# Kernel optimization log

Measured on AMD Instinct MI355X. Metric: run time of the kernel, lower is better.

The kernel has to match this reference:

```python
import jax, jax.numpy as jnp
import numpy as np

N = 50000      # nodes
E = 800000     # edges
IN = 128       # in_dim
EMB = 32       # emb_dim
ED = 8         # edge_dim
L = 4          # num_layers
B = 64         # num graphs in batch
OUT = 10       # out_dim
EPS = 1e-5


def setup_inputs() -> dict:
    key = jax.random.key(0)
    ks = jax.random.split(key, 16)
    f32 = jnp.float32
    def nrm(k, shape, scale):
        return jax.random.normal(k, shape, dtype=f32) * scale
    inp = {}
    inp['x'] = nrm(ks[0], (N, IN), 1.0)
    inp['edge_index'] = jax.random.randint(ks[1], (2, E), 0, N)
    inp['edge_attr'] = nrm(ks[2], (E, ED), 1.0)
    inp['batch'] = jnp.sort(jax.random.randint(ks[3], (N,), 0, B))
    # lin_in
    inp['lin_in_w'] = nrm(ks[4], (IN, EMB), 0.05)
    inp['lin_in_b'] = jnp.zeros((EMB,), f32)
    # per-layer message MLP: Linear(2e+ed->e), BN, ReLU, Linear(e->e), BN, ReLU
    inp['msg_w1'] = nrm(ks[5], (L, 2 * EMB + ED, EMB), 0.1)
    inp['msg_b1'] = jnp.zeros((L, EMB), f32)
    inp['msg_g1'] = jnp.ones((L, EMB), f32)
    inp['msg_be1'] = jnp.zeros((L, EMB), f32)
    inp['msg_w2'] = nrm(ks[6], (L, EMB, EMB), 0.1)
    inp['msg_b2'] = jnp.zeros((L, EMB), f32)
    inp['msg_g2'] = jnp.ones((L, EMB), f32)
    inp['msg_be2'] = jnp.zeros((L, EMB), f32)
    # per-layer update MLP: Linear(2e->e), BN, ReLU, Linear(e->e), BN, ReLU
    inp['upd_w1'] = nrm(ks[7], (L, 2 * EMB, EMB), 0.1)
    inp['upd_b1'] = jnp.zeros((L, EMB), f32)
    inp['upd_g1'] = jnp.ones((L, EMB), f32)
    inp['upd_be1'] = jnp.zeros((L, EMB), f32)
    inp['upd_w2'] = nrm(ks[8], (L, EMB, EMB), 0.1)
    inp['upd_b2'] = jnp.zeros((L, EMB), f32)
    inp['upd_g2'] = jnp.ones((L, EMB), f32)
    inp['upd_be2'] = jnp.zeros((L, EMB), f32)
    # lin_pred
    inp['pred_w'] = nrm(ks[9], (EMB, OUT), 0.1)
    inp['pred_b'] = jnp.zeros((OUT,), f32)
    return inp


def _bn(x, g, b):
    # BatchNorm1d in training mode: batch stats over dim 0 (biased variance)
    mu = jnp.mean(x, axis=0)
    var = jnp.mean(jnp.square(x - mu), axis=0)
    return (x - mu) * jax.lax.rsqrt(var + EPS) * g + b


def reference(x, edge_attr, lin_in_w, lin_in_b,
              msg_w1, msg_b1, msg_g1, msg_be1, msg_w2, msg_b2, msg_g2, msg_be2,
              upd_w1, upd_b1, upd_g1, upd_be1, upd_w2, upd_b2, upd_g2, upd_be2,
              pred_w, pred_b, edge_index, batch):
    src = edge_index[0]  # h_j source nodes
    dst = edge_index[1]  # h_i target nodes (aggregation index)
    h = x @ lin_in_w + lin_in_b  # [N, EMB]
    for i in range(L):
        # message: gather + concat + MLP(BN,ReLU)x2 over edges
        msg_in = jnp.concatenate([h[dst], h[src], edge_attr], axis=-1)  # [E, 2e+ed]
        m = jax.nn.relu(_bn(msg_in @ msg_w1[i] + msg_b1[i], msg_g1[i], msg_be1[i]))
        m = jax.nn.relu(_bn(m @ msg_w2[i] + msg_b2[i], msg_g2[i], msg_be2[i]))
        # aggregate: scatter-add by destination
        aggr = jax.ops.segment_sum(m, dst, num_segments=N)  # [N, EMB]
        # update: concat + MLP(BN,ReLU)x2
        u = jnp.concatenate([h, aggr], axis=-1)  # [N, 2e]
        u = jax.nn.relu(_bn(u @ upd_w1[i] + upd_b1[i], upd_g1[i], upd_be1[i]))
        u = jax.nn.relu(_bn(u @ upd_w2[i] + upd_b2[i], upd_g2[i], upd_be2[i]))
        h = u + h  # residual in MPNNModel.get_embeddings
    # global mean pool
    sums = jax.ops.segment_sum(h, batch, num_segments=B)
    counts = jax.ops.segment_sum(jnp.ones((N,), h.dtype), batch, num_segments=B)
    h_graph = sums / jnp.maximum(counts, 1.0)[:, None]
    return h_graph @ pred_w + pred_b  # [B, OUT]
```

## Files before the change

### kernel.cpp

```cpp
#include <hip/hip_runtime.h>
#include <cstddef>

#define N_NODES 50000
#define N_EDGES 800000
#define IN_DIM  128
#define EMB     32
#define ED      8
#define NLAYERS 4
#define NB      64
#define OUTD    10
#define EPS_BN  1e-5f

#define EDGE_GRID 3125
#define NODE_GRID 196
#define NODE4_GRID 782
#define AU_GRID   6250
#define MSG1_EPT  2
#define MSG1_GRID 1563
#define NCHUNK    12500
#define MSG12_CPW 4
#define MSG12_GRID 782
#define NTILE_N   3125
#define LIN_GRID  782
#define SREP 4

typedef short bf16x8 __attribute__((ext_vector_type(8)));
typedef float f32x4  __attribute__((ext_vector_type(4)));


__device__ __forceinline__ unsigned short f2bf(float x) {
  union { float f; unsigned u; } v; v.f = x;
  unsigned b = v.u + 0x7FFFu + ((v.u >> 16) & 1u);
  return (unsigned short)(b >> 16);
}
__device__ __forceinline__ float bf2f(unsigned short s) {
  union { unsigned u; float f; } v; v.u = ((unsigned)s) << 16;
  return v.f;
}

__device__ __forceinline__ void coef_from_stats(const float* __restrict__ stats_stage,
                                                const float* __restrict__ g,
                                                const float* __restrict__ be,
                                                float inv_count, float* __restrict__ cf) {
  if (threadIdx.x < EMB) {
    const int c = threadIdx.x;
    float s = 0.f, ss = 0.f;
#pragma unroll
    for (int r = 0; r < SREP; ++r) {
      s  += stats_stage[r*64 + c];
      ss += stats_stage[r*64 + EMB + c];
    }
    const float mu  = s * inv_count;
    const float var = ss * inv_count - mu*mu;
    const float a = g[c] * rsqrtf(var + EPS_BN);
    cf[c] = a;
    cf[EMB + c] = fmaf(-mu, a, be[c]);
  }
  __syncthreads();
}

__device__ __forceinline__ void block_stats_atomic(const float ts[EMB], const float tss[EMB],
                                                   float* __restrict__ stats_stage) {
  __shared__ float sred[256];
  const int lane = threadIdx.x & 63;
  const int wid  = threadIdx.x >> 6;
#pragma unroll
  for (int c = 0; c < EMB; ++c) {
    float a = ts[c];
    float q = tss[c];
#pragma unroll
    for (int o = 32; o > 0; o >>= 1) {
      a += __shfl_down(a, o, 64);
      q += __shfl_down(q, o, 64);
    }
    if (lane == 0) { sred[wid*64 + c] = a; sred[wid*64 + EMB + c] = q; }
  }
  __syncthreads();
  if (threadIdx.x < 64) {
    const float v = sred[threadIdx.x] + sred[64 + threadIdx.x] +
                    sred[128 + threadIdx.x] + sred[192 + threadIdx.x];
    atomicAdd(stats_stage + ((blockIdx.x & (SREP-1)) << 6) + threadIdx.x, v);
  }
}

__device__ __forceinline__ void wave_stats_atomic(float ts[8], float tss[8],
                                                  float* __restrict__ lds_s,
                                                  float* __restrict__ lds_q,
                                                  float* __restrict__ stats_stage) {
  const int lane = threadIdx.x & 63;
  const int wv   = threadIdx.x >> 6;
#pragma unroll
  for (int j = 0; j < 8; ++j) {
    float a = ts[j], b = tss[j];
#pragma unroll
    for (int o = 32; o > 0; o >>= 1) {
      a += __shfl_down(a, o, 64);
      b += __shfl_down(b, o, 64);
    }
    ts[j] = a; tss[j] = b;
  }
  if (lane == 0) {
#pragma unroll
    for (int j = 0; j < 8; ++j) {
      lds_s[wv*8 + j] = ts[j];
      lds_q[wv*8 + j] = tss[j];
    }
  }
  __syncthreads();
  if (threadIdx.x < 64) {
    const float v = (threadIdx.x < 32) ? lds_s[threadIdx.x] : lds_q[threadIdx.x - 32];
    atomicAdd(stats_stage + ((blockIdx.x & (SREP-1)) << 6) + threadIdx.x, v);
  }
}

__device__ __forceinline__ void y1_compute(float acc[EMB],
    const unsigned short* __restrict__ pb, const unsigned short* __restrict__ qb,
    int dst, int src, const unsigned short* __restrict__ ea_perm, int i,
    const float* __restrict__ w1b) {
  const uint4* pd = (const uint4*)(pb + (size_t)dst*EMB);
  const uint4* qs = (const uint4*)(qb + (size_t)src*EMB);
#pragma unroll
  for (int j4 = 0; j4 < 4; ++j4) {
    const uint4 a = pd[j4];
    const uint4 b = qs[j4];
    const unsigned ua[4] = {a.x, a.y, a.z, a.w};
    const unsigned ub[4] = {b.x, b.y, b.z, b.w};
#pragma unroll
    for (int t = 0; t < 4; ++t) {
      acc[j4*8 + 2*t]   = bf2f((unsigned short)(ua[t] & 0xFFFFu)) +
                          bf2f((unsigned short)(ub[t] & 0xFFFFu));
      acc[j4*8 + 2*t+1] = bf2f((unsigned short)(ua[t] >> 16)) +
                          bf2f((unsigned short)(ub[t] >> 16));
    }
  }
  const uint4 eraw = *(const uint4*)(ea_perm + (size_t)i*ED);
  const unsigned ue[4] = {eraw.x, eraw.y, eraw.z, eraw.w};
  float ev[8];
#pragma unroll
  for (int t = 0; t < 4; ++t) {
    ev[2*t]   = bf2f((unsigned short)(ue[t] & 0xFFFFu));
    ev[2*t+1] = bf2f((unsigned short)(ue[t] >> 16));
  }
#pragma unroll
  for (int k = 0; k < 8; ++k) {
    const float* wk = w1b + k*EMB;
#pragma unroll
    for (int c = 0; c < EMB; ++c) acc[c] = fmaf(ev[k], wk[c], acc[c]);
  }
}

#define HSTRIDE 40

__global__ __launch_bounds__(256) void k_lin_in_pq(
    const float* __restrict__ x, const float* __restrict__ w, const float* __restrict__ b,
    const float* __restrict__ w1, const float* __restrict__ b1, const int* __restrict__ ei,
    float* __restrict__ h, unsigned short* __restrict__ p, unsigned short* __restrict__ q,
    int* __restrict__ cnt)
{
  __shared__ __align__(16) unsigned short lds_hb[4][16*HSTRIDE];
  __shared__ __align__(16) unsigned short lds_pq[4][16*HSTRIDE];
  const int lane = threadIdx.x & 63;
  const int wv   = threadIdx.x >> 6;
  const int n0i  = lane & 15;
  const int quad = lane >> 4;

  const int tile = blockIdx.x*4 + wv;
  if (tile < NTILE_N) {
    const int r0 = tile*16;
    bf16x8 BwL[4], BwH[4];
#pragma unroll
    for (int kb = 0; kb < 4; ++kb) {
#pragma unroll
      for (int j = 0; j < 8; ++j) {
        const int k = kb*32 + quad*8 + j;
        BwL[kb][j] = (short)f2bf(w[k*EMB + n0i]);
        BwH[kb][j] = (short)f2bf(w[k*EMB + 16 + n0i]);
      }
    }
    f32x4 accL = {0.f,0.f,0.f,0.f};
    f32x4 accH = {0.f,0.f,0.f,0.f};
#pragma unroll
    for (int kb = 0; kb < 4; ++kb) {
      const float4 xa = *(const float4*)(x + (size_t)(r0 + n0i)*IN_DIM + kb*32 + quad*8);
      const float4 xb = *(const float4*)(x + (size_t)(r0 + n0i)*IN_DIM + kb*32 + quad*8 + 4);
      bf16x8 A;
      A[0] = (short)f2bf(xa.x); A[1] = (short)f2bf(xa.y);
      A[2] = (short)f2bf(xa.z); A[3] = (short)f2bf(xa.w);
      A[4] = (short)f2bf(xb.x); A[5] = (short)f2bf(xb.y);
      A[6] = (short)f2bf(xb.z); A[7] = (short)f2bf(xb.w);
      accL = __builtin_amdgcn_mfma_f32_16x16x32_bf16(A, BwL[kb], accL, 0, 0, 0);
      accH = __builtin_amdgcn_mfma_f32_16x16x32_bf16(A, BwH[kb], accH, 0, 0, 0);
    }
    const float bL = b[n0i], bH = b[16 + n0i];
#pragma unroll
    for (int r = 0; r < 4; ++r) {
      const int row = quad*4 + r;
      const float vL = accL[r] + bL;
      const float vH = accH[r] + bH;
      h[(size_t)(r0 + row)*EMB + n0i]      = vL;
      h[(size_t)(r0 + row)*EMB + 16 + n0i] = vH;
      lds_hb[wv][row*HSTRIDE + n0i]      = f2bf(vL);
      lds_hb[wv][row*HSTRIDE + 16 + n0i] = f2bf(vH);
    }
    bf16x8 A2;
#pragma unroll
    for (int j = 0; j < 8; ++j)
      A2[j] = (short)lds_hb[wv][n0i*HSTRIDE + quad*8 + j];
    bf16x8 BpL, BpH, BqL, BqH;
#pragma unroll
    for (int j = 0; j < 8; ++j) {
      const int k = quad*8 + j;
      BpL[j] = (short)f2bf(w1[k*EMB + n0i]);
      BpH[j] = (short)f2bf(w1[k*EMB + 16 + n0i]);
      BqL[j] = (short)f2bf(w1[(EMB + k)*EMB + n0i]);
      BqH[j] = (short)f2bf(w1[(EMB + k)*EMB + 16 + n0i]);
    }
    const f32x4 z4 = {0.f,0.f,0.f,0.f};
    f32x4 pL = __builtin_amdgcn_mfma_f32_16x16x32_bf16(A2, BpL, z4, 0, 0, 0);
    f32x4 pH = __builtin_amdgcn_mfma_f32_16x16x32_bf16(A2, BpH, z4, 0, 0, 0);
    f32x4 qL = __builtin_amdgcn_mfma_f32_16x16x32_bf16(A2, BqL, z4, 0, 0, 0);
    f32x4 qH = __builtin_amdgcn_mfma_f32_16x16x32_bf16(A2, BqH, z4, 0, 0, 0);
    const float b1L = b1[n0i], b1H = b1[16 + n0i];
#pragma unroll
    for (int r = 0; r < 4; ++r) {
      const int row = quad*4 + r;
      lds_pq[wv][row*HSTRIDE + n0i]      = f2bf(pL[r] + b1L);
      lds_pq[wv][row*HSTRIDE + 16 + n0i] = f2bf(pH[r] + b1H);
    }
    {
      const int row2 = lane >> 2;
      const int c8   = (lane & 3)*8;
      const uint4 ov = *(const uint4*)&lds_pq[wv][row2*HSTRIDE + c8];
      *(uint4*)(p + (size_t)(r0 + row2)*EMB + c8) = ov;
    }
#pragma unroll
    for (int r = 0; r < 4; ++r) {
      const int row = quad*4 + r;
      lds_pq[wv][row*HSTRIDE + n0i]      = f2bf(qL[r]);
      lds_pq[wv][row*HSTRIDE + 16 + n0i] = f2bf(qH[r]);
    }
    {
      const int row2 = lane >> 2;
      const int c8   = (lane & 3)*8;
      const uint4 ov = *(const uint4*)&lds_pq[wv][row2*HSTRIDE + c8];
      *(uint4*)(q + (size_t)(r0 + row2)*EMB + c8) = ov;
    }
  }
  for (int e = blockIdx.x*256 + threadIdx.x; e < N_EDGES; e += gridDim.x*256)
    atomicAdd(&cnt[ei[N_EDGES + e]], 1);
}

__global__ __launch_bounds__(256) void k_scan_a(const int* __restrict__ cnt,
                                                int* __restrict__ row_ptr, int* __restrict__ bsum) {
  __shared__ int s[256];
  const int gid = blockIdx.x*256 + threadIdx.x;
  const int v = (gid < N_NODES) ? cnt[gid] : 0;
  s[threadIdx.x] = v;
  __syncthreads();
  for (int o = 1; o < 256; o <<= 1) {
    const int t = (threadIdx.x >= o) ? s[threadIdx.x - o] : 0;
    __syncthreads();
    s[threadIdx.x] += t;
    __syncthreads();
  }
  if (gid < N_NODES) row_ptr[gid] = s[threadIdx.x] - v;
  if (threadIdx.x == 255) bsum[blockIdx.x] = s[255];
}

__global__ __launch_bounds__(256) void k_scan_bc(int* __restrict__ row_ptr,
                                                 const int* __restrict__ bsum) {
  __shared__ int s[256];
  const int t = threadIdx.x;
  const int v = (t < NODE_GRID) ? bsum[t] : 0;
  s[t] = v;
  __syncthreads();
  for (int o = 1; o < 256; o <<= 1) {
    const int tt = (t >= o) ? s[t - o] : 0;
    __syncthreads();
    s[t] += tt;
    __syncthreads();
  }
  const int off = (blockIdx.x == 0) ? 0 : s[blockIdx.x - 1];
  const int gid = blockIdx.x*256 + t;
  if (gid < N_NODES) row_ptr[gid] += off;
  if (blockIdx.x == 0 && t == 0) row_ptr[N_NODES] = N_EDGES;
}

__global__ __launch_bounds__(256) void k_place(const int* __restrict__ ei,
                                               const int* __restrict__ row_ptr,
                                               int* __restrict__ cnt2, int* __restrict__ perm) {
  const int e = blockIdx.x*256 + threadIdx.x;
  const int d = ei[N_EDGES + e];
  const int pos = row_ptr[d] + atomicAdd(&cnt2[d], 1);
  perm[pos] = e;
}

__global__ __launch_bounds__(256) void k_permute(
    const int* __restrict__ perm, const int* __restrict__ ei, const float* __restrict__ ea,
    int* __restrict__ src_perm, int* __restrict__ dst_perm, unsigned short* __restrict__ ea_perm)
{
  const int i = blockIdx.x*256 + threadIdx.x;
  const int e = perm[i];
  src_perm[i] = ei[e];
  dst_perm[i] = ei[N_EDGES + e];
  const float4 v0 = ((const float4*)(ea + (size_t)e*ED))[0];
  const float4 v1 = ((const float4*)(ea + (size_t)e*ED))[1];
  const float ev[8] = {v0.x, v0.y, v0.z, v0.w, v1.x, v1.y, v1.z, v1.w};
  unsigned u[4];
#pragma unroll
  for (int j = 0; j < 4; ++j)
    u[j] = (unsigned)f2bf(ev[2*j]) | ((unsigned)f2bf(ev[2*j+1]) << 16);
  uint4 o; o.x = u[0]; o.y = u[1]; o.z = u[2]; o.w = u[3];
  *(uint4*)(ea_perm + (size_t)i*ED) = o;
}


__global__ __launch_bounds__(256) void k_msg1_stats(
    const unsigned short* __restrict__ pb, const unsigned short* __restrict__ qb,
    const int* __restrict__ src_perm, const int* __restrict__ dst_perm,
    const unsigned short* __restrict__ ea_perm,
    const float* __restrict__ w1b, float* __restrict__ stats)
{
  float ts[EMB], tss[EMB];
#pragma unroll
  for (int c = 0; c < EMB; ++c) { ts[c] = 0.f; tss[c] = 0.f; }
  const int base = blockIdx.x*(256*MSG1_EPT) + threadIdx.x;
  for (int it = 0; it < MSG1_EPT; ++it) {
    const int i = base + it*256;
    if (i >= N_EDGES) break;
    float acc[EMB];
    y1_compute(acc, pb, qb, dst_perm[i], src_perm[i], ea_perm, i, w1b);
#pragma unroll
    for (int c = 0; c < EMB; ++c) {
      ts[c] += acc[c];
      tss[c] = fmaf(acc[c], acc[c], tss[c]);
    }
  }
  block_stats_atomic(ts, tss, stats);
}

#define MSTRIDE 40
__global__ __launch_bounds__(256) void k_msg12(
    const unsigned short* __restrict__ pb, const unsigned short* __restrict__ qb,
    const int* __restrict__ src_perm, const int* __restrict__ dst_perm,
    const unsigned short* __restrict__ ea_perm,
    const float* __restrict__ w1b,
    const float* __restrict__ stats1, const float* __restrict__ g1, const float* __restrict__ be1,
    const float* __restrict__ w2, const float* __restrict__ b2,
    unsigned short* __restrict__ y, float* __restrict__ stats2)
{
  __shared__ __align__(16) unsigned short lds_a[4][64*MSTRIDE];
  __shared__ float lds_s[4][32], lds_q[4][32];
  __shared__ float cf[64];

  coef_from_stats(stats1, g1, be1, 1.0f/(float)N_EDGES, cf);

  const int lane = threadIdx.x & 63;
  const int wv   = threadIdx.x >> 6;
  const int n0i  = lane & 15;
  const int kb   = lane >> 4;

  bf16x8 Blo, Bhi;
#pragma unroll
  for (int j = 0; j < 8; ++j) {
    Blo[j] = (short)f2bf(w2[(kb*8 + j)*EMB + n0i]);
    Bhi[j] = (short)f2bf(w2[(kb*8 + j)*EMB + 16 + n0i]);
  }
  const float b2c0 = b2[n0i], b2c1 = b2[16 + n0i];
  float a1[EMB], c1[EMB];
#pragma unroll
  for (int c = 0; c < EMB; ++c) { a1[c] = cf[c]; c1[c] = cf[EMB + c]; }

  float ts[8], tss[8];
#pragma unroll
  for (int j = 0; j < 8; ++j) { ts[j] = 0.f; tss[j] = 0.f; }

  const int chunk0 = (blockIdx.x*4 + wv)*MSG12_CPW;
  for (int cix = 0; cix < MSG12_CPW; ++cix) {
    const int chunk = chunk0 + cix;
    if (chunk >= NCHUNK) break;
    const size_t e0 = (size_t)chunk*64;
    const int i = (int)e0 + lane;

    {
      float acc[EMB];
      y1_compute(acc, pb, qb, dst_perm[i], src_perm[i], ea_perm, i, w1b);
      unsigned u[16];
#pragma unroll
      for (int j = 0; j < 16; ++j) {
        const float v0 = fmaxf(fmaf(a1[2*j],   acc[2*j],   c1[2*j]),   0.f);
        const float v1 = fmaxf(fmaf(a1[2*j+1], acc[2*j+1], c1[2*j+1]), 0.f);
        u[j] = (unsigned)f2bf(v0) | ((unsigned)f2bf(v1) << 16);
      }
      uint4* row = (uint4*)&lds_a[wv][lane*MSTRIDE];
#pragma unroll
      for (int j = 0; j < 4; ++j) {
        uint4 o; o.x = u[4*j]; o.y = u[4*j+1]; o.z = u[4*j+2]; o.w = u[4*j+3];
        row[j] = o;
      }
    }
#pragma unroll
    for (int t = 0; t < 4; ++t) {
      const uint4 araw = *(const uint4*)&lds_a[wv][(16*t + n0i)*MSTRIDE + kb*8];
      bf16x8 A;
      const unsigned ua[4] = {araw.x, araw.y, araw.z, araw.w};
#pragma unroll
      for (int j = 0; j < 4; ++j) {
        A[2*j]   = (short)(ua[j] & 0xFFFFu);
        A[2*j+1] = (short)(ua[j] >> 16);
      }
      f32x4 acc0 = {0.f, 0.f, 0.f, 0.f};
      f32x4 acc1 = {0.f, 0.f, 0.f, 0.f};
      acc0 = __builtin_amdgcn_mfma_f32_16x16x32_bf16(A, Blo, acc0, 0, 0, 0);
      acc1 = __builtin_amdgcn_mfma_f32_16x16x32_bf16(A, Bhi, acc1, 0, 0, 0);
#pragma unroll
      for (int r = 0; r < 4; ++r) {
        const int row = 16*t + kb*4 + r;
        lds_a[wv][row*MSTRIDE + n0i]      = f2bf(acc0[r] + b2c0);
        lds_a[wv][row*MSTRIDE + 16 + n0i] = f2bf(acc1[r] + b2c1);
      }
    }
#pragma unroll
    for (int j = 0; j < 4; ++j) {
      const int c64 = lane + 64*j;
      const int row = c64 >> 2;
      const int c8  = (c64 & 3)*8;
      const uint4 ov = *(const uint4*)&lds_a[wv][row*MSTRIDE + c8];
      *(uint4*)(y + (e0 + row)*EMB + c8) = ov;
      const unsigned uo[4] = {ov.x, ov.y, ov.z, ov.w};
#pragma unroll
      for (int jj = 0; jj < 4; ++jj) {
        const float v0 = bf2f((unsigned short)(uo[jj] & 0xFFFFu));
        const float v1 = bf2f((unsigned short)(uo[jj] >> 16));
        ts[2*jj]   += v0;  tss[2*jj]   = fmaf(v0, v0, tss[2*jj]);
        ts[2*jj+1] += v1;  tss[2*jj+1] = fmaf(v1, v1, tss[2*jj+1]);
      }
    }
  }

#pragma unroll
  for (int j = 0; j < 8; ++j) {
    float s = ts[j], qq = tss[j];
#pragma unroll
    for (int o = 4; o < 64; o <<= 1) {
      s  += __shfl_xor(s, o, 64);
      qq += __shfl_xor(qq, o, 64);
    }
    ts[j] = s; tss[j] = qq;
  }
  if (lane < 4) {
#pragma unroll
    for (int j = 0; j < 8; ++j) {
      lds_s[wv][lane*8 + j] = ts[j];
      lds_q[wv][lane*8 + j] = tss[j];
    }
  }
  __syncthreads();
  if (threadIdx.x < 64) {
    const int c = threadIdx.x & 31;
    const int kind = threadIdx.x >> 5;
    float v = 0.f;
#pragma unroll
    for (int wq = 0; wq < 4; ++wq)
      v += kind ? lds_q[wq][c] : lds_s[wq][c];
    atomicAdd(stats2 + ((blockIdx.x & (SREP-1)) << 6) + kind*32 + c, v);
  }
}

__global__ __launch_bounds__(256) void k_aggr_upd1(
    const unsigned short* __restrict__ y, const int* __restrict__ row_ptr,
    const float* __restrict__ h,
    const float* __restrict__ stats1, const float* __restrict__ g2, const float* __restrict__ be2,
    const float* __restrict__ uw1, const float* __restrict__ ub1,
    float* __restrict__ z, float* __restrict__ stats2)
{
  __shared__ float cf[64];
  __shared__ float lh[8][32];
  __shared__ float la[8][32];
  __shared__ float rs[4][32], rq[4][32];
  coef_from_stats(stats1, g2, be2, 1.0f/(float)N_EDGES, cf);

  const int g = threadIdx.x >> 5;
  const int l = threadIdx.x & 31;
  const int n = blockIdx.x*8 + g;

  lh[g][l] = h[(size_t)n*EMB + l];

  const int rof = l >> 4;
  const int cp  = l & 15;
  const float a0 = cf[2*cp],     b0 = cf[EMB + 2*cp];
  const float a1 = cf[2*cp + 1], b1 = cf[EMB + 2*cp + 1];
  const int lo = row_ptr[n], hi = row_ptr[n+1];
  float s0 = 0.f, s1 = 0.f;
  for (int i = lo + rof; i < hi; i += 2) {
    const unsigned u = *(const unsigned*)(y + (size_t)i*EMB + 2*cp);
    const float v0 = bf2f((unsigned short)(u & 0xFFFFu));
    const float v1 = bf2f((unsigned short)(u >> 16));
    s0 += fmaxf(fmaf(a0, v0, b0), 0.f);
    s1 += fmaxf(fmaf(a1, v1, b1), 0.f);
  }
  s0 += __shfl_xor(s0, 16, 64);
  s1 += __shfl_xor(s1, 16, 64);
  if (rof == 0) { la[g][2*cp] = s0; la[g][2*cp + 1] = s1; }
  __syncthreads();

  float acc = ub1[l];
#pragma unroll
  for (int k = 0; k < EMB; ++k) acc = fmaf(lh[g][k], uw1[k*EMB + l], acc);
#pragma unroll
  for (int k = 0; k < EMB; ++k) acc = fmaf(la[g][k], uw1[(EMB + k)*EMB + l], acc);
  z[(size_t)n*EMB + l] = acc;

  const float sq = acc*acc;
  const float a2 = acc + __shfl_down(acc, 32, 64);
  const float q2 = sq  + __shfl_down(sq,  32, 64);
  const int wv = threadIdx.x >> 6;
  if ((threadIdx.x & 63) < 32) { rs[wv][l] = a2; rq[wv][l] = q2; }
  __syncthreads();
  if (threadIdx.x < 64) {
    const int c = threadIdx.x & 31;
    const int kind = threadIdx.x >> 5;
    float v = 0.f;
#pragma unroll
    for (int wq = 0; wq < 4; ++wq)
      v += kind ? rq[wq][c] : rs[wq][c];
    atomicAdd(stats2 + ((blockIdx.x & (SREP-1)) << 6) + kind*32 + c, v);
  }
}

__global__ __launch_bounds__(256) void k_upd2(
    float* __restrict__ z,
    const float* __restrict__ stats1, const float* __restrict__ g1, const float* __restrict__ be1,
    const float* __restrict__ w, const float* __restrict__ b,
    float* __restrict__ stats2)
{
  __shared__ float cf[64];
  __shared__ float lds_s[32], lds_q[32];
  coef_from_stats(stats1, g1, be1, 1.0f/(float)N_NODES, cf);

  const int lane = threadIdx.x & 63;
  const int wv   = threadIdx.x >> 6;
  const int n  = blockIdx.x*64 + lane;
  const int c0 = wv*8;
  float acc[8];
#pragma unroll
  for (int j = 0; j < 8; ++j) acc[j] = 0.f;
  if (n < N_NODES) {
#pragma unroll
    for (int j = 0; j < 8; ++j) acc[j] = b[c0 + j];
    const float4* zp = (const float4*)(z + (size_t)n*EMB);
#pragma unroll
    for (int k4 = 0; k4 < 8; ++k4) {
      const float4 v = zp[k4];
      const float mv[4] = {v.x, v.y, v.z, v.w};
#pragma unroll
      for (int t = 0; t < 4; ++t) {
        const int k = 4*k4 + t;
        const float m = fmaxf(fmaf(cf[k], mv[t], cf[EMB + k]), 0.f);
        const float* wk = w + k*EMB + c0;
#pragma unroll
        for (int j = 0; j < 8; ++j) acc[j] = fmaf(m, wk[j], acc[j]);
      }
    }
  }
  float ts[8], tss[8];
#pragma unroll
  for (int j = 0; j < 8; ++j) { ts[j] = acc[j]; tss[j] = acc[j]*acc[j]; }
  wave_stats_atomic(ts, tss, lds_s, lds_q, stats2);
  if (n < N_NODES) {
    float4 o0, o1;
    o0.x = acc[0]; o0.y = acc[1]; o0.z = acc[2]; o0.w = acc[3];
    o1.x = acc[4]; o1.y = acc[5]; o1.z = acc[6]; o1.w = acc[7];
    *(float4*)(z + (size_t)n*EMB + c0)     = o0;
    *(float4*)(z + (size_t)n*EMB + c0 + 4) = o1;
  }
}

__global__ __launch_bounds__(256) void k_resid_pq(
    float* __restrict__ h, const float* __restrict__ z,
    const float* __restrict__ stats, const float* __restrict__ g, const float* __restrict__ be,
    const float* __restrict__ w1_next, const float* __restrict__ b1_next,
    unsigned short* __restrict__ p, unsigned short* __restrict__ q)
{
  __shared__ float cf[64];
  __shared__ float lds_h[64][33];
  coef_from_stats(stats, g, be, 1.0f/(float)N_NODES, cf);

  const int lane = threadIdx.x & 63;
  const int wv   = threadIdx.x >> 6;
  const int n  = blockIdx.x*64 + lane;
  const int c0 = wv*8;
  if (n < N_NODES) {
    const float4* zp = (const float4*)(z + (size_t)n*EMB + c0);
    float4* hp = (float4*)(h + (size_t)n*EMB + c0);
    float hn[8];
    const float4 z0 = zp[0], z1 = zp[1];
    const float4 h0 = hp[0], h1 = hp[1];
    const float zv[8] = {z0.x, z0.y, z0.z, z0.w, z1.x, z1.y, z1.z, z1.w};
    const float hv[8] = {h0.x, h0.y, h0.z, h0.w, h1.x, h1.y, h1.z, h1.w};
#pragma unroll
    for (int j = 0; j < 8; ++j) {
      const int k = c0 + j;
      hn[j] = hv[j] + fmaxf(fmaf(cf[k], zv[j], cf[EMB + k]), 0.f);
      lds_h[lane][k] = hn[j];
    }
    float4 o0, o1;
    o0.x = hn[0]; o0.y = hn[1]; o0.z = hn[2]; o0.w = hn[3];
    o1.x = hn[4]; o1.y = hn[5]; o1.z = hn[6]; o1.w = hn[7];
    hp[0] = o0; hp[1] = o1;
  }
  __syncthreads();
  if (n < N_NODES && w1_next) {
    float ap[8], aq[8];
#pragma unroll
    for (int j = 0; j < 8; ++j) { ap[j] = b1_next[c0 + j]; aq[j] = 0.f; }
#pragma unroll
    for (int k = 0; k < EMB; ++k) {
      const float hvv = lds_h[lane][k];
      const float* wp = w1_next + k*EMB + c0;
      const float* wq = w1_next + (EMB + k)*EMB + c0;
#pragma unroll
      for (int j = 0; j < 8; ++j) ap[j] = fmaf(hvv, wp[j], ap[j]);
#pragma unroll
      for (int j = 0; j < 8; ++j) aq[j] = fmaf(hvv, wq[j], aq[j]);
    }
    unsigned up[4], uq[4];
#pragma unroll
    for (int j = 0; j < 4; ++j) {
      up[j] = (unsigned)f2bf(ap[2*j]) | ((unsigned)f2bf(ap[2*j+1]) << 16);
      uq[j] = (unsigned)f2bf(aq[2*j]) | ((unsigned)f2bf(aq[2*j+1]) << 16);
    }
    uint4 op; op.x = up[0]; op.y = up[1]; op.z = up[2]; op.w = up[3];
    uint4 oq; oq.x = uq[0]; oq.y = uq[1]; oq.z = uq[2]; oq.w = uq[3];
    *(uint4*)(p + (size_t)n*EMB + c0) = op;
    *(uint4*)(q + (size_t)n*EMB + c0) = oq;
  }
}

__global__ void k_pool(const float* __restrict__ h, const int* __restrict__ batch,
                       const float* __restrict__ pw, const float* __restrict__ pb,
                       float* __restrict__ out)
{
  __shared__ float sred[256];
  __shared__ float hg[EMB];
  const int b = blockIdx.x;
  int lo = 0, hi = N_NODES;
  while (lo < hi) { int m = (lo + hi) >> 1; if (batch[m] < b) lo = m + 1; else hi = m; }
  const int start = lo;
  hi = N_NODES;
  while (lo < hi) { int m = (lo + hi) >> 1; if (batch[m] < b + 1) lo = m + 1; else hi = m; }
  const int end = lo;

  const int c = threadIdx.x & (EMB-1);
  const int r = threadIdx.x >> 5;
  float s = 0.f;
  for (int n = start + r; n < end; n += 8) s += h[(size_t)n*EMB + c];
  sred[threadIdx.x] = s;
  __syncthreads();
  if (threadIdx.x < EMB) {
    float tot = 0.f;
#pragma unroll
    for (int r2 = 0; r2 < 8; ++r2) tot += sred[r2*EMB + threadIdx.x];
    const float cnt = (float)(end - start);
    hg[threadIdx.x] = tot / fmaxf(cnt, 1.f);
  }
  __syncthreads();
  if (threadIdx.x < OUTD) {
    float acc = pb[threadIdx.x];
#pragma unroll
    for (int cc = 0; cc < EMB; ++cc) acc = fmaf(hg[cc], pw[cc*OUTD + threadIdx.x], acc);
    out[b*OUTD + threadIdx.x] = acc;
  }
}


extern "C" void kernel_launch(void* const* d_in, const int* in_sizes, int n_in,
                              void* d_out, int out_size, void* d_ws, size_t ws_size,
                              hipStream_t stream) {
  const float* x        = (const float*)d_in[0];
  const int*   ei       = (const int*)  d_in[1];
  const float* ea       = (const float*)d_in[2];
  const int*   batch    = (const int*)  d_in[3];
  const float* lin_in_w = (const float*)d_in[4];
  const float* lin_in_b = (const float*)d_in[5];
  const float* msg_w1   = (const float*)d_in[6];
  const float* msg_b1   = (const float*)d_in[7];
  const float* msg_g1   = (const float*)d_in[8];
  const float* msg_be1  = (const float*)d_in[9];
  const float* msg_w2   = (const float*)d_in[10];
  const float* msg_b2   = (const float*)d_in[11];
  const float* msg_g2   = (const float*)d_in[12];
  const float* msg_be2  = (const float*)d_in[13];
  const float* upd_w1   = (const float*)d_in[14];
  const float* upd_b1   = (const float*)d_in[15];
  const float* upd_g1   = (const float*)d_in[16];
  const float* upd_be1  = (const float*)d_in[17];
  const float* upd_w2   = (const float*)d_in[18];
  const float* upd_b2   = (const float*)d_in[19];
  const float* upd_g2   = (const float*)d_in[20];
  const float* upd_be2  = (const float*)d_in[21];
  const float* pred_w   = (const float*)d_in[22];
  const float* pred_b   = (const float*)d_in[23];
  float* out = (float*)d_out;

  char* wsb = (char*)d_ws;
  unsigned short* y  = (unsigned short*)wsb;
  unsigned short* eap= (unsigned short*)(wsb + (size_t)N_EDGES*EMB*2);
  unsigned short* p  = eap + (size_t)N_EDGES*ED;
  unsigned short* q  = p + (size_t)N_NODES*EMB;
  float* h       = (float*)(q + (size_t)N_NODES*EMB);
  float* z       = h + (size_t)N_NODES*EMB;
  float* stats   = z + (size_t)N_NODES*EMB;
  int*   cnt     = (int*)(stats + 16*SREP*64);
  int*   cnt2    = cnt + N_NODES;
  int*   row_ptr = cnt2 + N_NODES;
  int*   bsum    = row_ptr + N_NODES + 1;
  int*   perm    = bsum + 256;
  int*   src_perm= perm + N_EDGES;
  int*   dst_perm= src_perm + N_EDGES;
  const size_t need = ((size_t)((char*)(dst_perm + N_EDGES) - wsb));
  if (ws_size < need) return;

  hipMemsetAsync(stats, 0, (16*SREP*64 + 2*N_NODES)*sizeof(float), stream);

  k_lin_in_pq<<<LIN_GRID, 256, 0, stream>>>(x, lin_in_w, lin_in_b, msg_w1, msg_b1, ei,
                                            h, p, q, cnt);
  k_scan_a<<<NODE_GRID, 256, 0, stream>>>(cnt, row_ptr, bsum);
  k_scan_bc<<<NODE_GRID, 256, 0, stream>>>(row_ptr, bsum);
  k_place<<<EDGE_GRID, 256, 0, stream>>>(ei, row_ptr, cnt2, perm);
  k_permute<<<EDGE_GRID, 256, 0, stream>>>(perm, ei, ea, src_perm, dst_perm, eap);

  for (int l = 0; l < NLAYERS; ++l) {
    const int st = l*4;
    const float* w1  = msg_w1 + (size_t)l*(2*EMB+ED)*EMB;
    const float* w1b = w1 + (size_t)2*EMB*EMB;
    const float* w2  = msg_w2 + (size_t)l*EMB*EMB;
    const float* uw1 = upd_w1 + (size_t)l*(2*EMB)*EMB;
    const float* uw2 = upd_w2 + (size_t)l*EMB*EMB;
    const float* w1_next = (l+1 < NLAYERS) ? msg_w1 + (size_t)(l+1)*(2*EMB+ED)*EMB : nullptr;
    const float* b1_next = (l+1 < NLAYERS) ? msg_b1 + (size_t)(l+1)*EMB : nullptr;

    k_msg1_stats<<<MSG1_GRID, 256, 0, stream>>>(p, q, src_perm, dst_perm, eap,
                                                w1b, stats + (size_t)st*SREP*64);
    k_msg12<<<MSG12_GRID, 256, 0, stream>>>(p, q, src_perm, dst_perm, eap, w1b,
                                            stats + (size_t)st*SREP*64,
                                            msg_g1 + l*EMB, msg_be1 + l*EMB,
                                            w2, msg_b2 + l*EMB,
                                            y, stats + (size_t)(st+1)*SREP*64);
    k_aggr_upd1<<<AU_GRID, 256, 0, stream>>>(y, row_ptr, h,
                                             stats + (size_t)(st+1)*SREP*64,
                                             msg_g2 + l*EMB, msg_be2 + l*EMB,
                                             uw1, upd_b1 + l*EMB,
                                             z, stats + (size_t)(st+2)*SREP*64);
    k_upd2<<<NODE4_GRID, 256, 0, stream>>>(z, stats + (size_t)(st+2)*SREP*64,
                                           upd_g1 + l*EMB, upd_be1 + l*EMB,
                                           uw2, upd_b2 + l*EMB, stats + (size_t)(st+3)*SREP*64);
    k_resid_pq<<<NODE4_GRID, 256, 0, stream>>>(h, z, stats + (size_t)(st+3)*SREP*64,
                                               upd_g2 + l*EMB, upd_be2 + l*EMB,
                                               w1_next, b1_next, p, q);
  }

  k_pool<<<NB, 256, 0, stream>>>(h, batch, pred_w, pred_b, out);
}
```

Baseline: 906.9 us.

## Process edges in original order and scatter message rows by CSR rank

Drops the permute pass that built dst-sorted src/dst/edge-attr arrays. Instead each edge gets a rank (its CSR slot), and the message kernels read edges in original order, then scatter each output row of y to its rank position. This removes one setup kernel and the permuted index arrays. In exchange, the node gathers in the message kernels lose the locality that dst-sorted order gave, and y writes become scattered 64-byte rows.

New measurement: 920.0 us. Within noise of the previous version (+1.4%).

```diff
diff --git a/kernel.cpp b/kernel.cpp
--- a/kernel.cpp
+++ b/kernel.cpp
@@ -115,7 +115,7 @@
 
 __device__ __forceinline__ void y1_compute(float acc[EMB],
     const unsigned short* __restrict__ pb, const unsigned short* __restrict__ qb,
-    int dst, int src, const unsigned short* __restrict__ ea_perm, int i,
+    int dst, int src, const unsigned short* __restrict__ eab, int e,
     const float* __restrict__ w1b) {
   const uint4* pd = (const uint4*)(pb + (size_t)dst*EMB);
   const uint4* qs = (const uint4*)(qb + (size_t)src*EMB);
@@ -133,7 +133,7 @@
                           bf2f((unsigned short)(ub[t] >> 16));
     }
   }
-  const uint4 eraw = *(const uint4*)(ea_perm + (size_t)i*ED);
+  const uint4 eraw = *(const uint4*)(eab + (size_t)e*ED);
   const unsigned ue[4] = {eraw.x, eraw.y, eraw.z, eraw.w};
   float ev[8];
 #pragma unroll
@@ -286,23 +286,14 @@
   if (blockIdx.x == 0 && t == 0) row_ptr[N_NODES] = N_EDGES;
 }
 
-__global__ __launch_bounds__(256) void k_place(const int* __restrict__ ei,
-                                               const int* __restrict__ row_ptr,
-                                               int* __restrict__ cnt2, int* __restrict__ perm) {
+__global__ __launch_bounds__(256) void k_rank_ea(
+    const int* __restrict__ ei, const float* __restrict__ ea,
+    const int* __restrict__ row_ptr, int* __restrict__ cnt2,
+    int* __restrict__ rank, unsigned short* __restrict__ eab)
+{
   const int e = blockIdx.x*256 + threadIdx.x;
   const int d = ei[N_EDGES + e];
-  const int pos = row_ptr[d] + atomicAdd(&cnt2[d], 1);
-  perm[pos] = e;
-}
-
-__global__ __launch_bounds__(256) void k_permute(
-    const int* __restrict__ perm, const int* __restrict__ ei, const float* __restrict__ ea,
-    int* __restrict__ src_perm, int* __restrict__ dst_perm, unsigned short* __restrict__ ea_perm)
-{
-  const int i = blockIdx.x*256 + threadIdx.x;
-  const int e = perm[i];
-  src_perm[i] = ei[e];
-  dst_perm[i] = ei[N_EDGES + e];
+  rank[e] = row_ptr[d] + atomicAdd(&cnt2[d], 1);
   const float4 v0 = ((const float4*)(ea + (size_t)e*ED))[0];
   const float4 v1 = ((const float4*)(ea + (size_t)e*ED))[1];
   const float ev[8] = {v0.x, v0.y, v0.z, v0.w, v1.x, v1.y, v1.z, v1.w};
@@ -311,14 +302,13 @@
   for (int j = 0; j < 4; ++j)
     u[j] = (unsigned)f2bf(ev[2*j]) | ((unsigned)f2bf(ev[2*j+1]) << 16);
   uint4 o; o.x = u[0]; o.y = u[1]; o.z = u[2]; o.w = u[3];
-  *(uint4*)(ea_perm + (size_t)i*ED) = o;
+  *(uint4*)(eab + (size_t)e*ED) = o;
 }
 
 
 __global__ __launch_bounds__(256) void k_msg1_stats(
     const unsigned short* __restrict__ pb, const unsigned short* __restrict__ qb,
-    const int* __restrict__ src_perm, const int* __restrict__ dst_perm,
-    const unsigned short* __restrict__ ea_perm,
+    const int* __restrict__ ei, const unsigned short* __restrict__ eab,
     const float* __restrict__ w1b, float* __restrict__ stats)
 {
   float ts[EMB], tss[EMB];
@@ -326,10 +316,10 @@
   for (int c = 0; c < EMB; ++c) { ts[c] = 0.f; tss[c] = 0.f; }
   const int base = blockIdx.x*(256*MSG1_EPT) + threadIdx.x;
   for (int it = 0; it < MSG1_EPT; ++it) {
-    const int i = base + it*256;
-    if (i >= N_EDGES) break;
+    const int e = base + it*256;
+    if (e >= N_EDGES) break;
     float acc[EMB];
-    y1_compute(acc, pb, qb, dst_perm[i], src_perm[i], ea_perm, i, w1b);
+    y1_compute(acc, pb, qb, ei[N_EDGES + e], ei[e], eab, e, w1b);
 #pragma unroll
     for (int c = 0; c < EMB; ++c) {
       ts[c] += acc[c];
@@ -342,11 +332,11 @@
 #define MSTRIDE 40
 __global__ __launch_bounds__(256) void k_msg12(
     const unsigned short* __restrict__ pb, const unsigned short* __restrict__ qb,
-    const int* __restrict__ src_perm, const int* __restrict__ dst_perm,
-    const unsigned short* __restrict__ ea_perm,
+    const int* __restrict__ ei, const unsigned short* __restrict__ eab,
     const float* __restrict__ w1b,
     const float* __restrict__ stats1, const float* __restrict__ g1, const float* __restrict__ be1,
     const float* __restrict__ w2, const float* __restrict__ b2,
+    const int* __restrict__ rank,
     unsigned short* __restrict__ y, float* __restrict__ stats2)
 {
   __shared__ __align__(16) unsigned short lds_a[4][64*MSTRIDE];
@@ -380,11 +370,11 @@
     const int chunk = chunk0 + cix;
     if (chunk >= NCHUNK) break;
     const size_t e0 = (size_t)chunk*64;
-    const int i = (int)e0 + lane;
+    const int e = (int)e0 + lane;
 
     {
       float acc[EMB];
-      y1_compute(acc, pb, qb, dst_perm[i], src_perm[i], ea_perm, i, w1b);
+      y1_compute(acc, pb, qb, ei[N_EDGES + e], ei[e], eab, e, w1b);
       unsigned u[16];
 #pragma unroll
       for (int j = 0; j < 16; ++j) {
@@ -425,8 +415,9 @@
       const int c64 = lane + 64*j;
       const int row = c64 >> 2;
       const int c8  = (c64 & 3)*8;
+      const int pos = rank[(int)e0 + row];
       const uint4 ov = *(const uint4*)&lds_a[wv][row*MSTRIDE + c8];
-      *(uint4*)(y + (e0 + row)*EMB + c8) = ov;
+      *(uint4*)(y + (size_t)pos*EMB + c8) = ov;
       const unsigned uo[4] = {ov.x, ov.y, ov.z, ov.w};
 #pragma unroll
       for (int jj = 0; jj < 4; ++jj) {
@@ -705,8 +696,8 @@
 
   char* wsb = (char*)d_ws;
   unsigned short* y  = (unsigned short*)wsb;
-  unsigned short* eap= (unsigned short*)(wsb + (size_t)N_EDGES*EMB*2);
-  unsigned short* p  = eap + (size_t)N_EDGES*ED;
+  unsigned short* eab= (unsigned short*)(wsb + (size_t)N_EDGES*EMB*2);
+  unsigned short* p  = eab + (size_t)N_EDGES*ED;
   unsigned short* q  = p + (size_t)N_NODES*EMB;
   float* h       = (float*)(q + (size_t)N_NODES*EMB);
   float* z       = h + (size_t)N_NODES*EMB;
@@ -715,10 +706,8 @@
   int*   cnt2    = cnt + N_NODES;
   int*   row_ptr = cnt2 + N_NODES;
   int*   bsum    = row_ptr + N_NODES + 1;
-  int*   perm    = bsum + 256;
-  int*   src_perm= perm + N_EDGES;
-  int*   dst_perm= src_perm + N_EDGES;
-  const size_t need = ((size_t)((char*)(dst_perm + N_EDGES) - wsb));
+  int*   rank    = bsum + 256;
+  const size_t need = ((size_t)((char*)(rank + N_EDGES) - wsb));
   if (ws_size < need) return;
 
   hipMemsetAsync(stats, 0, (16*SREP*64 + 2*N_NODES)*sizeof(float), stream);
@@ -727,8 +716,7 @@
                                             h, p, q, cnt);
   k_scan_a<<<NODE_GRID, 256, 0, stream>>>(cnt, row_ptr, bsum);
   k_scan_bc<<<NODE_GRID, 256, 0, stream>>>(row_ptr, bsum);
-  k_place<<<EDGE_GRID, 256, 0, stream>>>(ei, row_ptr, cnt2, perm);
-  k_permute<<<EDGE_GRID, 256, 0, stream>>>(perm, ei, ea, src_perm, dst_perm, eap);
+  k_rank_ea<<<EDGE_GRID, 256, 0, stream>>>(ei, ea, row_ptr, cnt2, rank, eab);
 
   for (int l = 0; l < NLAYERS; ++l) {
     const int st = l*4;
@@ -740,12 +728,12 @@
     const float* w1_next = (l+1 < NLAYERS) ? msg_w1 + (size_t)(l+1)*(2*EMB+ED)*EMB : nullptr;
     const float* b1_next = (l+1 < NLAYERS) ? msg_b1 + (size_t)(l+1)*EMB : nullptr;
 
-    k_msg1_stats<<<MSG1_GRID, 256, 0, stream>>>(p, q, src_perm, dst_perm, eap,
-                                                w1b, stats + (size_t)st*SREP*64);
-    k_msg12<<<MSG12_GRID, 256, 0, stream>>>(p, q, src_perm, dst_perm, eap, w1b,
+    k_msg1_stats<<<MSG1_GRID, 256, 0, stream>>>(p, q, ei, eab, w1b,
+                                                stats + (size_t)st*SREP*64);
+    k_msg12<<<MSG12_GRID, 256, 0, stream>>>(p, q, ei, eab, w1b,
                                             stats + (size_t)st*SREP*64,
                                             msg_g1 + l*EMB, msg_be1 + l*EMB,
-                                            w2, msg_b2 + l*EMB,
+                                            w2, msg_b2 + l*EMB, rank,
                                             y, stats + (size_t)(st+1)*SREP*64);
     k_aggr_upd1<<<AU_GRID, 256, 0, stream>>>(y, row_ptr, h,
                                              stats + (size_t)(st+1)*SREP*64,
```
